# Optimization experiments

Measured on AMD Instinct MI355X. Metric: run time of the kernel, lower is better.

Reference implementation:

```python
import jax, jax.numpy as jnp
import numpy as np

DIM = 2048
HEADS = 16
KV_HEADS = 4
DIM_HEAD = 128
INNER = HEADS * DIM_HEAD          # 2048
KV_INNER = KV_HEADS * DIM_HEAD    # 512
FF = 4 * DIM                      # 8192
QK_SCALE = 10.0                   # x-transformers default qk_norm_scale
B, S = 2, 2048


def layer_norm(x, g, b, eps=1e-5):
    m = jnp.mean(x, axis=-1, keepdims=True)
    v = jnp.mean((x - m) ** 2, axis=-1, keepdims=True)
    return (x - m) * jax.lax.rsqrt(v + eps) * g + b


def l2norm(t, eps=1e-12):
    n = jnp.sqrt(jnp.sum(t * t, axis=-1, keepdims=True))
    return t / jnp.maximum(n, eps)


def setup_inputs() -> dict:
    key = jax.random.key(0)
    ks = jax.random.split(key, 12)
    s = lambda fan_in: 1.0 / np.sqrt(fan_in)
    return {
        "x":     jax.random.normal(ks[0], (B, S, DIM), jnp.float32),
        "wq":    jax.random.normal(ks[1], (DIM, INNER), jnp.float32) * s(DIM),
        "wk":    jax.random.normal(ks[2], (DIM, KV_INNER), jnp.float32) * s(DIM),
        "wv":    jax.random.normal(ks[3], (DIM, KV_INNER), jnp.float32) * s(DIM),
        "wo":    jax.random.normal(ks[4], (INNER, DIM), jnp.float32) * s(INNER),
        "ln1_g": jnp.ones((DIM,), jnp.float32),
        "ln1_b": jnp.zeros((DIM,), jnp.float32),
        "w1":    jax.random.normal(ks[5], (DIM, FF), jnp.float32) * s(DIM),
        "b1":    jnp.zeros((FF,), jnp.float32),
        "lnf_g": jnp.ones((FF,), jnp.float32),
        "lnf_b": jnp.zeros((FF,), jnp.float32),
        "w2":    jax.random.normal(ks[6], (FF, DIM), jnp.float32) * s(FF),
        "b2":    jnp.zeros((DIM,), jnp.float32),
    }


def reference(x, wq, wk, wv, wo, ln1_g, ln1_b, w1, b1, lnf_g, lnf_b, w2, b2):
    b, s, _ = x.shape
    rep = HEADS // KV_HEADS
    # GQA projections
    q = (x @ wq).reshape(b, s, HEADS, DIM_HEAD).transpose(0, 2, 1, 3)      # [b,h,s,d]
    k = (x @ wk).reshape(b, s, KV_HEADS, DIM_HEAD).transpose(0, 2, 1, 3)   # [b,g,s,d]
    v = (x @ wv).reshape(b, s, KV_HEADS, DIM_HEAD).transpose(0, 2, 1, 3)
    # qk-norm: l2-normalize q/k along head dim, fixed scale
    q = l2norm(q)
    k = l2norm(k)
    k = jnp.repeat(k, rep, axis=1)  # expand kv heads to query heads
    v = jnp.repeat(v, rep, axis=1)
    scores = jnp.einsum("bhid,bhjd->bhij", q, k) * QK_SCALE
    attn = jax.nn.softmax(scores, axis=-1)
    o = jnp.einsum("bhij,bhjd->bhid", attn, v)
    o = o.transpose(0, 2, 1, 3).reshape(b, s, INNER) @ wo
    # post-attention LayerNorm (no residual in the source)
    h = layer_norm(o, ln1_g, ln1_b)
    # FFN: SiLU + post-activation LayerNorm (dropout inert in eval)
    f = jax.nn.silu(h @ w1 + b1)
    f = layer_norm(f, lnf_g, lnf_b)
    y = f @ w2 + b2
    # the source re-applies the SAME norm after the ffn
    return layer_norm(y, ln1_g, ln1_b)
```

## Files before the change

### kernel.cpp

```cpp
#include <hip/hip_runtime.h>


typedef __attribute__((ext_vector_type(8))) short short8;
typedef __attribute__((ext_vector_type(4))) float f32x4;
typedef __attribute__((ext_vector_type(16))) float f32x16;

__device__ __forceinline__ unsigned short f2bf(float f) {
  unsigned int u = __builtin_bit_cast(unsigned int, f);
  u += 0x7FFFu + ((u >> 16) & 1u);
  return (unsigned short)(u >> 16);
}
__device__ __forceinline__ float bf2f(unsigned short h) {
  unsigned int u = ((unsigned int)h) << 16;
  return __builtin_bit_cast(float, u);
}

typedef const void __attribute__((address_space(1)))* gas1_t;
typedef void __attribute__((address_space(3)))* las3_t;
#define GLDS16(g, l) \
  __builtin_amdgcn_global_load_lds((gas1_t)(const void*)(g), (las3_t)(void*)(l), 16, 0, 0)

__global__ __launch_bounds__(256) void cast_f32_bf16(const float* __restrict__ src,
                                                     unsigned short* __restrict__ dst,
                                                     int n) {
  int i = (blockIdx.x * 256 + threadIdx.x) * 4;
  if (i >= n) return;
  float4 f = *(const float4*)(src + i);
  uint2 u;
  u.x = (unsigned)f2bf(f.x) | ((unsigned)f2bf(f.y) << 16);
  u.y = (unsigned)f2bf(f.z) | ((unsigned)f2bf(f.w) << 16);
  *(uint2*)(dst + i) = u;
}

__global__ void transcast(const float* __restrict__ src, unsigned short* __restrict__ dst,
                          int R, int C, int dst_ld, int row_off) {
  __shared__ float t[32][33];
  const int tx = threadIdx.x, ty = threadIdx.y;
  const int c0 = blockIdx.x * 32, r0 = blockIdx.y * 32;
#pragma unroll
  for (int j = 0; j < 4; ++j)
    t[ty + j * 8][tx] = src[(size_t)(r0 + ty + j * 8) * C + c0 + tx];
  __syncthreads();
#pragma unroll
  for (int j = 0; j < 4; ++j)
    dst[(size_t)(row_off + c0 + ty + j * 8) * dst_ld + r0 + tx] = f2bf(t[tx][ty + j * 8]);
}

template <int BN>
__global__ __launch_bounds__(512, 2) void gemm256(const unsigned short* __restrict__ A,
                                                  const unsigned short* __restrict__ Bt,
                                                  unsigned short* __restrict__ C,
                                                  int M, int N, int K) {
  constexpr int NF = BN / 64;
  constexpr int HB = BN * 64;
  constexpr int RB = BN / 128;
  constexpr int AK1 = 16384 + HB;
  constexpr int BUFB = 32768 + 2 * HB;
  extern __shared__ char lds[];

  const int tid = threadIdx.x, l = tid & 63, w = tid >> 6;
  const int wr = w >> 2, wc = w & 3;
  const int brow = blockIdx.y * 256, bcol = blockIdx.x * BN;
  const unsigned short* Aa = A + (size_t)brow * K;
  const unsigned short* Bb = Bt + (size_t)bcol * K;
  const int NT = K >> 6;

  const int slot = l >> 4;
  const int rowA = wr * 128 + (l & 15);
  const int aRd = ((((rowA << 2) | slot) << 4) ^ ((rowA & 7) << 4));
  const int rowB = wc * (BN / 4) + (l & 15);
  const int bRd = ((((rowB << 2) | slot) << 4) ^ ((rowB & 7) << 4));

  f32x4 acc[8][NF];
#pragma unroll
  for (int m = 0; m < 8; ++m)
#pragma unroll
    for (int n = 0; n < NF; ++n) acc[m][n] = (f32x4){0.f, 0.f, 0.f, 0.f};

  auto stageA = [&](char* dst, int kofs) {
#pragma unroll
    for (int r = 0; r < 2; ++r) {
      const int g = r * 512 + tid;
      const int rw = ((g >> 3) << 1) | (((g >> 2) ^ (g >> 4)) & 1);
      const int sl = (g ^ rw) & 3;
      GLDS16(Aa + (size_t)rw * K + kofs + sl * 8, dst + g * 16);
    }
  };
  auto stageB = [&](char* dst, int kofs) {
#pragma unroll
    for (int r = 0; r < RB; ++r) {
      const int g = r * 512 + tid;
      const int rw = ((g >> 3) << 1) | (((g >> 2) ^ (g >> 4)) & 1);
      const int sl = (g ^ rw) & 3;
      GLDS16(Bb + (size_t)rw * K + kofs + sl * 8, dst + g * 16);
    }
  };

  stageA(lds, 0);
  stageB(lds + 16384, 0);
  stageA(lds + AK1, 32);
  stageB(lds + AK1 + 16384, 32);

  int kt = 0;
  for (int t = 0; t < NT; ++t) {
    char* curb = lds + (t & 1) * BUFB;
    char* nxtb = lds + ((t & 1) ^ 1) * BUFB;
    const int ktn = (t + 1 < NT) ? kt + 64 : 0;
    short8 af[4], bf[NF];

    if constexpr (BN == 256) asm volatile("s_waitcnt vmcnt(4)" ::: "memory");
    else                     asm volatile("s_waitcnt vmcnt(3)" ::: "memory");
    asm volatile("s_barrier" ::: "memory");
#pragma unroll
    for (int n = 0; n < NF; ++n) bf[n] = *(const short8*)(curb + 16384 + bRd + n * 1024);
#pragma unroll
    for (int m = 0; m < 4; ++m) af[m] = *(const short8*)(curb + aRd + m * 1024);
    stageA(nxtb, ktn);
    __builtin_amdgcn_s_setprio(1);
#pragma unroll
    for (int m = 0; m < 4; ++m)
#pragma unroll
      for (int n = 0; n < NF; ++n)
        acc[m][n] = __builtin_amdgcn_mfma_f32_16x16x32_bf16(af[m], bf[n], acc[m][n], 0, 0, 0);
    __builtin_amdgcn_s_setprio(0);

    asm volatile("s_barrier" ::: "memory");
#pragma unroll
    for (int m = 0; m < 4; ++m) af[m] = *(const short8*)(curb + aRd + (m + 4) * 1024);
    stageB(nxtb + 16384, ktn);
    __builtin_amdgcn_s_setprio(1);
#pragma unroll
    for (int m = 0; m < 4; ++m)
#pragma unroll
      for (int n = 0; n < NF; ++n)
        acc[m + 4][n] = __builtin_amdgcn_mfma_f32_16x16x32_bf16(af[m], bf[n], acc[m + 4][n], 0, 0, 0);
    __builtin_amdgcn_s_setprio(0);

    if constexpr (BN == 256) asm volatile("s_waitcnt vmcnt(4)" ::: "memory");
    else                     asm volatile("s_waitcnt vmcnt(3)" ::: "memory");
    asm volatile("s_barrier" ::: "memory");
#pragma unroll
    for (int n = 0; n < NF; ++n) bf[n] = *(const short8*)(curb + AK1 + 16384 + bRd + n * 1024);
#pragma unroll
    for (int m = 0; m < 4; ++m) af[m] = *(const short8*)(curb + AK1 + aRd + m * 1024);
    stageA(nxtb + AK1, ktn + 32);
    __builtin_amdgcn_s_setprio(1);
#pragma unroll
    for (int m = 0; m < 4; ++m)
#pragma unroll
      for (int n = 0; n < NF; ++n)
        acc[m][n] = __builtin_amdgcn_mfma_f32_16x16x32_bf16(af[m], bf[n], acc[m][n], 0, 0, 0);
    __builtin_amdgcn_s_setprio(0);

    asm volatile("s_barrier" ::: "memory");
#pragma unroll
    for (int m = 0; m < 4; ++m) af[m] = *(const short8*)(curb + AK1 + aRd + (m + 4) * 1024);
    stageB(nxtb + AK1 + 16384, ktn + 32);
    __builtin_amdgcn_s_setprio(1);
#pragma unroll
    for (int m = 0; m < 4; ++m)
#pragma unroll
      for (int n = 0; n < NF; ++n)
        acc[m + 4][n] = __builtin_amdgcn_mfma_f32_16x16x32_bf16(af[m], bf[n], acc[m + 4][n], 0, 0, 0);
    __builtin_amdgcn_s_setprio(0);

    kt += 64;
  }

#pragma unroll
  for (int m = 0; m < 8; ++m)
#pragma unroll
    for (int r = 0; r < 4; ++r) {
      const int row = brow + wr * 128 + m * 16 + (l >> 4) * 4 + r;
#pragma unroll
      for (int n = 0; n < NF; ++n) {
        const int col = bcol + wc * (BN / 4) + n * 16 + (l & 15);
        C[(size_t)row * N + col] = f2bf(acc[m][n][r]);
      }
    }
}

__global__ __launch_bounds__(256) void l2norm_qk(unsigned short* __restrict__ qkv) {
  const int wid = blockIdx.x * 4 + (threadIdx.x >> 6);
  const int l = threadIdx.x & 63;
  const int token = wid / 20, u = wid % 20;
  const int col = (u < 16) ? u * 128 : 2048 + (u - 16) * 128;
  unsigned short* p = qkv + (size_t)token * 3072 + col + l * 2;
  const float a = bf2f(p[0]), b = bf2f(p[1]);
  float ss = a * a + b * b;
#pragma unroll
  for (int m = 1; m < 64; m <<= 1) ss += __shfl_xor(ss, m);
  const float sc = ((u < 16) ? 10.f : 1.f) / fmaxf(sqrtf(ss), 1e-12f);
  p[0] = f2bf(a * sc);
  p[1] = f2bf(b * sc);
}

__global__ __launch_bounds__(256) void vtrans(const unsigned short* __restrict__ qkv,
                                              unsigned short* __restrict__ vt) {
  const int idx = blockIdx.x * 256 + threadIdx.x;
  const int s_ = idx & 2047;
  const int rest = idx >> 11;
  const int d = rest & 127;
  const int bg = rest >> 7;
  const int b = bg >> 2, g = bg & 3;
  vt[idx] = qkv[(size_t)(b * 2048 + s_) * 3072 + 2560 + g * 128 + d];
}

__global__ __launch_bounds__(512) void attn_kernel(const unsigned short* __restrict__ qkv,
                                                   const unsigned short* __restrict__ vt,
                                                   unsigned short* __restrict__ out) {
  extern __shared__ char smem[];
  const int tid = threadIdx.x, w = tid >> 6, l = tid & 63;
  const int hi = l >> 5, l31 = l & 31;

  const int n = blockIdx.x;
  const int np = (n & 7) * 32 + (n >> 3);
  const int qi = np & 7, bh = np >> 3;
  const int b = bh >> 4, h = bh & 15, g = h >> 2;
  const int q0 = qi * 256;

  const unsigned short* kbase = qkv + (size_t)(b * 2048) * 3072 + 2048 + g * 128;
  const unsigned short* vbase = vt + (size_t)(b * 4 + g) * 128 * 2048;

  short8 qf[8];
  {
    const unsigned short* qrow = qkv + (size_t)(b * 2048 + q0 + w * 32 + l31) * 3072 + h * 128;
#pragma unroll
    for (int st = 0; st < 8; ++st)
      qf[st] = *(const short8*)&qrow[st * 16 + hi * 8];
  }

  f32x16 o[4];
#pragma unroll
  for (int d0 = 0; d0 < 4; ++d0)
#pragma unroll
    for (int i = 0; i < 16; ++i) o[d0][i] = 0.f;
  float l_part = 0.f;

  const int krow = tid >> 3, kc = (tid & 7) * 2;
  const int vd = tid >> 2, vc = (tid & 3) * 2;
  const unsigned short* kg = kbase + (size_t)krow * 3072 + kc * 8;
  const unsigned short* vg = vbase + (size_t)vd * 2048 + vc * 8;
  const int ko0 = krow * 256 + ((kc ^ (krow & 15)) << 4);
  const int ko1 = krow * 256 + (((kc + 1) ^ (krow & 15)) << 4);
  const int vrp = vd >> 1, vcl = (vd & 1) * 8;
  const int vo0 = vrp * 256 + (((vcl + vc) ^ (vrp & 15)) << 4);
  const int vo1 = vrp * 256 + (((vcl + vc + 1) ^ (vrp & 15)) << 4);

  {
    uint4 k0 = *(const uint4*)kg, k1 = *(const uint4*)(kg + 8);
    uint4 v0 = *(const uint4*)vg, v1 = *(const uint4*)(vg + 8);
    char* Kb = smem;
    char* Vb = smem + 16384;
    *(uint4*)(Kb + ko0) = k0; *(uint4*)(Kb + ko1) = k1;
    *(uint4*)(Vb + vo0) = v0; *(uint4*)(Vb + vo1) = v1;
  }
  __syncthreads();

  const int swzk = l31 & 15;
  for (int t = 0; t < 32; ++t) {
    uint4 k0, k1, v0, v1;
    const bool more = (t + 1) < 32;
    if (more) {
      const size_t kvo = (size_t)(t + 1) * 64;
      k0 = *(const uint4*)(kg + kvo * 3072);
      k1 = *(const uint4*)(kg + kvo * 3072 + 8);
      v0 = *(const uint4*)(vg + kvo);
      v1 = *(const uint4*)(vg + kvo + 8);
    }

    char* Kb = smem + (t & 1) * 32768;
    char* Vb = Kb + 16384;

    f32x16 s0, s1;
#pragma unroll
    for (int i = 0; i < 16; ++i) { s0[i] = 0.f; s1[i] = 0.f; }
    __builtin_amdgcn_s_setprio(1);
#pragma unroll
    for (int st = 0; st < 8; ++st) {
      const int ch = st * 2 + hi;
      short8 kf0 = *(const short8*)(Kb + l31 * 256 + ((ch ^ swzk) << 4));
      short8 kf1 = *(const short8*)(Kb + (l31 + 32) * 256 + ((ch ^ swzk) << 4));
      s0 = __builtin_amdgcn_mfma_f32_32x32x16_bf16(kf0, qf[st], s0, 0, 0, 0);
      s1 = __builtin_amdgcn_mfma_f32_32x32x16_bf16(kf1, qf[st], s1, 0, 0, 0);
    }
    __builtin_amdgcn_s_setprio(0);

#pragma unroll
    for (int i = 0; i < 16; ++i) {
      s0[i] = __expf(s0[i] - 10.f);
      s1[i] = __expf(s1[i] - 10.f);
      l_part += s0[i] + s1[i];
    }

    short8 pa[4];
#pragma unroll
    for (int ks = 0; ks < 4; ++ks) {
      const f32x16& sv = (ks < 2) ? s0 : s1;
      const int base = (ks & 1) * 8;
      auto pk = [](float x, float y) -> unsigned {
        unsigned ux = __builtin_bit_cast(unsigned, x);
        unsigned uy = __builtin_bit_cast(unsigned, y);
        return ((uy + 0x8000u) & 0xFFFF0000u) | ((ux + 0x8000u) >> 16);
      };
      unsigned a = pk(sv[base + 0], sv[base + 1]);
      unsigned bq = pk(sv[base + 4], sv[base + 5]);
      unsigned c = pk(sv[base + 2], sv[base + 3]);
      unsigned d = pk(sv[base + 6], sv[base + 7]);
      unsigned as = __shfl_xor(a, 32), bs = __shfl_xor(bq, 32);
      unsigned cs = __shfl_xor(c, 32), ds = __shfl_xor(d, 32);
      uint4 wv;
      wv.x = (l < 32) ? a : bs;
      wv.y = (l < 32) ? c : ds;
      wv.z = (l < 32) ? as : bq;
      wv.w = (l < 32) ? cs : d;
      pa[ks] = __builtin_bit_cast(short8, wv);
    }

    __builtin_amdgcn_s_setprio(1);
#pragma unroll
    for (int ks = 0; ks < 4; ++ks) {
#pragma unroll
      for (int d0 = 0; d0 < 4; ++d0) {
        const int dd = d0 * 32 + l31;
        const int rp = dd >> 1;
        const int cl = ((dd & 1) * 8 + ks * 2 + hi) ^ (rp & 15);
        short8 vf = *(const short8*)(Vb + rp * 256 + (cl << 4));
        o[d0] = __builtin_amdgcn_mfma_f32_32x32x16_bf16(pa[ks], vf, o[d0], 0, 0, 0);
      }
    }
    __builtin_amdgcn_s_setprio(0);

    __syncthreads();
    if (more) {
      char* Kn = smem + ((t + 1) & 1) * 32768;
      char* Vn = Kn + 16384;
      *(uint4*)(Kn + ko0) = k0; *(uint4*)(Kn + ko1) = k1;
      *(uint4*)(Vn + vo0) = v0; *(uint4*)(Vn + vo1) = v1;
    }
    __syncthreads();
  }

  float ltot = l_part + __shfl_xor(l_part, 32);
  float linv = 1.f / ltot;
  const int tok_base = b * 2048 + q0 + w * 32;
#pragma unroll
  for (int r = 0; r < 16; ++r) {
    const int qr = (r & 3) + 8 * (r >> 2) + 4 * hi;
    const float li = __shfl(linv, qr);
    unsigned short* orow = out + (size_t)(tok_base + qr) * 2048 + h * 128 + l31;
#pragma unroll
    for (int d0 = 0; d0 < 4; ++d0)
      orow[d0 * 32] = f2bf(o[d0][r] * li);
  }
}

template <int NC, bool BIAS, bool SILU, bool OUTF32>
__global__ __launch_bounds__(256) void ln_row(const unsigned short* __restrict__ src,
                                              unsigned short* __restrict__ dstb,
                                              float* __restrict__ dstf,
                                              const float* __restrict__ gamma,
                                              const float* __restrict__ beta,
                                              const float* __restrict__ bias) {
  constexpr int E = NC / 256;
  const int row = blockIdx.x, tid = threadIdx.x;
  const size_t base = (size_t)row * NC + tid * E;
  float v[E];
#pragma unroll
  for (int c = 0; c < E / 8; ++c) {
    uint4 u = *(const uint4*)(src + base + c * 8);
    const unsigned short* us = (const unsigned short*)&u;
#pragma unroll
    for (int j = 0; j < 8; ++j) v[c * 8 + j] = bf2f(us[j]);
  }
  if constexpr (BIAS) {
#pragma unroll
    for (int i = 0; i < E; ++i) v[i] += bias[tid * E + i];
  }
  if constexpr (SILU) {
#pragma unroll
    for (int i = 0; i < E; ++i) v[i] = v[i] / (1.f + __expf(-v[i]));
  }
  float s = 0.f, q = 0.f;
#pragma unroll
  for (int i = 0; i < E; ++i) {
    s += v[i];
    q += v[i] * v[i];
  }
#pragma unroll
  for (int m = 1; m < 64; m <<= 1) {
    s += __shfl_xor(s, m);
    q += __shfl_xor(q, m);
  }
  __shared__ float rs[4], rq[4];
  if ((tid & 63) == 0) {
    rs[tid >> 6] = s;
    rq[tid >> 6] = q;
  }
  __syncthreads();
  s = rs[0] + rs[1] + rs[2] + rs[3];
  q = rq[0] + rq[1] + rq[2] + rq[3];
  const float mean = s / NC;
  const float rstd = rsqrtf(q / NC - mean * mean + 1e-5f);
#pragma unroll
  for (int i = 0; i < E; ++i)
    v[i] = (v[i] - mean) * rstd * gamma[tid * E + i] + beta[tid * E + i];
  if constexpr (OUTF32) {
#pragma unroll
    for (int c = 0; c < E / 4; ++c) {
      float4 f = {v[c * 4], v[c * 4 + 1], v[c * 4 + 2], v[c * 4 + 3]};
      *(float4*)(dstf + base + c * 4) = f;
    }
  } else {
#pragma unroll
    for (int c = 0; c < E / 8; ++c) {
      uint4 u;
      unsigned* up = (unsigned*)&u;
#pragma unroll
      for (int j = 0; j < 4; ++j)
        up[j] = (unsigned)f2bf(v[c * 8 + j * 2]) | ((unsigned)f2bf(v[c * 8 + j * 2 + 1]) << 16);
      *(uint4*)(dstb + base + c * 8) = u;
    }
  }
}

extern "C" void kernel_launch(void* const* d_in, const int* in_sizes, int n_in,
                              void* d_out, int out_size, void* d_ws, size_t ws_size,
                              hipStream_t stream) {
  (void)in_sizes; (void)n_in; (void)out_size; (void)ws_size;
  const float* x     = (const float*)d_in[0];
  const float* wq    = (const float*)d_in[1];
  const float* wk    = (const float*)d_in[2];
  const float* wv    = (const float*)d_in[3];
  const float* wo    = (const float*)d_in[4];
  const float* ln1_g = (const float*)d_in[5];
  const float* ln1_b = (const float*)d_in[6];
  const float* w1    = (const float*)d_in[7];
  const float* b1    = (const float*)d_in[8];
  const float* lnf_g = (const float*)d_in[9];
  const float* lnf_b = (const float*)d_in[10];
  const float* w2    = (const float*)d_in[11];
  const float* b2    = (const float*)d_in[12];

  unsigned short* ws = (unsigned short*)d_ws;
  unsigned short* wqkvT  = ws;
  unsigned short* woT    = wqkvT  + (size_t)3072 * 2048;
  unsigned short* w1T    = woT    + (size_t)2048 * 2048;
  unsigned short* w2T    = w1T    + (size_t)8192 * 2048;
  unsigned short* xb     = w2T    + (size_t)2048 * 8192;
  unsigned short* qkv    = xb     + (size_t)4096 * 2048;
  unsigned short* vt     = qkv    + (size_t)4096 * 3072;
  unsigned short* attn_o = vt     + (size_t)4096 * 512;
  unsigned short* f1     = attn_o + (size_t)4096 * 2048;

  (void)hipFuncSetAttribute((const void*)gemm256<256>,
                            hipFuncAttributeMaxDynamicSharedMemorySize, 131072);
  (void)hipFuncSetAttribute((const void*)gemm256<128>,
                            hipFuncAttributeMaxDynamicSharedMemorySize, 98304);
  (void)hipFuncSetAttribute((const void*)attn_kernel,
                            hipFuncAttributeMaxDynamicSharedMemorySize, 65536);

  const dim3 tb(32, 8);
  cast_f32_bf16<<<8192, 256, 0, stream>>>(x, xb, 4096 * 2048);
  transcast<<<dim3(64, 64),  tb, 0, stream>>>(wq, wqkvT, 2048, 2048, 2048, 0);
  transcast<<<dim3(16, 64),  tb, 0, stream>>>(wk, wqkvT, 2048, 512, 2048, 2048);
  transcast<<<dim3(16, 64),  tb, 0, stream>>>(wv, wqkvT, 2048, 512, 2048, 2560);
  transcast<<<dim3(64, 64),  tb, 0, stream>>>(wo, woT, 2048, 2048, 2048, 0);
  transcast<<<dim3(256, 64), tb, 0, stream>>>(w1, w1T, 2048, 8192, 2048, 0);
  transcast<<<dim3(64, 256), tb, 0, stream>>>(w2, w2T, 8192, 2048, 8192, 0);

  gemm256<256><<<dim3(12, 16), 512, 131072, stream>>>(xb, wqkvT, qkv, 4096, 3072, 2048);
  l2norm_qk<<<20480, 256, 0, stream>>>(qkv);
  vtrans<<<8192, 256, 0, stream>>>(qkv, vt);
  attn_kernel<<<256, 512, 65536, stream>>>(qkv, vt, attn_o);
  gemm256<128><<<dim3(16, 16), 512, 98304, stream>>>(attn_o, woT, xb, 4096, 2048, 2048);
  ln_row<2048, false, false, false><<<4096, 256, 0, stream>>>(xb, xb, nullptr, ln1_g, ln1_b, nullptr);
  gemm256<256><<<dim3(32, 16), 512, 131072, stream>>>(xb, w1T, f1, 4096, 8192, 2048);
  ln_row<8192, true, true, false><<<4096, 256, 0, stream>>>(f1, f1, nullptr, lnf_g, lnf_b, b1);
  gemm256<128><<<dim3(16, 16), 512, 98304, stream>>>(f1, w2T, qkv, 4096, 2048, 8192);
  ln_row<2048, true, false, true><<<4096, 256, 0, stream>>>(qkv, nullptr, (float*)d_out, ln1_g, ln1_b, b2);
}
```

Before: 651.3 us.

## Add triple-buffered 256x128 GEMM with XCD-aware tile mapping for N=2048 GEMMs

Adds a gemm128r3 kernel that uses three LDS buffers (144KB, one block per CU) to prefetch two K-steps ahead, and replaces gemm256<128> for the Wo and W2 projections with it. Both the new kernel and gemm256 now remap block IDs so that blocks sharing an XCD work on nearby tiles, to improve L2 reuse of A and B. The deeper pipeline hides global-load latency but halves occupancy relative to the 2-blocks-per-CU variant. The remap in gemm256 assumes the grid size is divisible by 8.

Measured after the change: 645.0 us. No clear change (-1.0%).

```diff
diff --git a/kernel.cpp b/kernel.cpp
--- a/kernel.cpp
+++ b/kernel.cpp
@@ -60,7 +60,11 @@
 
   const int tid = threadIdx.x, l = tid & 63, w = tid >> 6;
   const int wr = w >> 2, wc = w & 3;
-  const int brow = blockIdx.y * 256, bcol = blockIdx.x * BN;
+  const int gx = gridDim.x, gy = gridDim.y;
+  const int did = blockIdx.y * gx + blockIdx.x;
+  const int q = (gx * gy) >> 3;
+  const int tcm = (did & 7) * q + (did >> 3);
+  const int brow = (tcm % gy) * 256, bcol = (tcm / gy) * BN;
   const unsigned short* Aa = A + (size_t)brow * K;
   const unsigned short* Bb = Bt + (size_t)bcol * K;
   const int NT = K >> 6;
@@ -175,6 +179,135 @@
 #pragma unroll
       for (int n = 0; n < NF; ++n) {
         const int col = bcol + wc * (BN / 4) + n * 16 + (l & 15);
+        C[(size_t)row * N + col] = f2bf(acc[m][n][r]);
+      }
+    }
+}
+
+__global__ __launch_bounds__(512, 1) void gemm128r3(const unsigned short* __restrict__ A,
+                                                    const unsigned short* __restrict__ Bt,
+                                                    unsigned short* __restrict__ C,
+                                                    int M, int N, int K) {
+  constexpr int BUFB = 49152;
+  extern __shared__ char lds[];
+  const int tid = threadIdx.x, l = tid & 63, w = tid >> 6;
+  const int wr = w >> 2, wc = w & 3;
+  const int did = blockIdx.y * 16 + blockIdx.x;
+  const int xcd = did & 7, idx = did >> 3;
+  const int brow = ((xcd >> 1) * 4 + (idx & 3)) * 256;
+  const int bcol = ((xcd & 1) * 8 + (idx >> 2)) * 128;
+  const unsigned short* Aa = A + (size_t)brow * K;
+  const unsigned short* Bb = Bt + (size_t)bcol * K;
+  const int NT = K >> 6;
+
+  const int slot = l >> 4;
+  const int rowA = wr * 128 + (l & 15);
+  const int aRd = ((((rowA << 2) | slot) << 4) ^ ((rowA & 7) << 4));
+  const int rowB = wc * 32 + (l & 15);
+  const int bRd = ((((rowB << 2) | slot) << 4) ^ ((rowB & 7) << 4));
+
+  f32x4 acc[8][2];
+#pragma unroll
+  for (int m = 0; m < 8; ++m)
+#pragma unroll
+    for (int n = 0; n < 2; ++n) acc[m][n] = (f32x4){0.f, 0.f, 0.f, 0.f};
+
+  auto stageA = [&](char* dst, int kofs) {
+#pragma unroll
+    for (int r = 0; r < 2; ++r) {
+      const int g = r * 512 + tid;
+      const int rw = ((g >> 3) << 1) | (((g >> 2) ^ (g >> 4)) & 1);
+      const int sl = (g ^ rw) & 3;
+      GLDS16(Aa + (size_t)rw * K + kofs + sl * 8, dst + g * 16);
+    }
+  };
+  auto stageB = [&](char* dst, int kofs) {
+    const int g = tid;
+    const int rw = ((g >> 3) << 1) | (((g >> 2) ^ (g >> 4)) & 1);
+    const int sl = (g ^ rw) & 3;
+    GLDS16(Bb + (size_t)rw * K + kofs + sl * 8, dst + g * 16);
+  };
+
+  stageA(lds, 0);                  stageB(lds + 16384, 0);
+  stageA(lds + 24576, 32);         stageB(lds + 40960, 32);
+  stageA(lds + BUFB, 64);          stageB(lds + BUFB + 16384, 64);
+  stageA(lds + BUFB + 24576, 96);  stageB(lds + BUFB + 40960, 96);
+
+  char* b0 = lds;
+  char* b1 = lds + BUFB;
+  char* b2 = lds + 2 * BUFB;
+  int kt2 = 128;
+  for (int t = 0; t < NT; ++t) {
+    char* cur = b0;
+    char* nxt = b2;
+    const int kn = (t + 2 < NT) ? kt2 : 0;
+    short8 af[4], bf[2];
+
+    asm volatile("s_waitcnt vmcnt(6)" ::: "memory");
+    asm volatile("s_barrier" ::: "memory");
+    bf[0] = *(const short8*)(cur + 16384 + bRd);
+    bf[1] = *(const short8*)(cur + 16384 + bRd + 1024);
+#pragma unroll
+    for (int m = 0; m < 4; ++m) af[m] = *(const short8*)(cur + aRd + m * 1024);
+    stageA(nxt, kn);
+    stageB(nxt + 16384, kn);
+    __builtin_amdgcn_s_setprio(1);
+#pragma unroll
+    for (int m = 0; m < 4; ++m)
+#pragma unroll
+      for (int n = 0; n < 2; ++n)
+        acc[m][n] = __builtin_amdgcn_mfma_f32_16x16x32_bf16(af[m], bf[n], acc[m][n], 0, 0, 0);
+    __builtin_amdgcn_s_setprio(0);
+
+    asm volatile("s_barrier" ::: "memory");
+#pragma unroll
+    for (int m = 0; m < 4; ++m) af[m] = *(const short8*)(cur + aRd + (m + 4) * 1024);
+    stageA(nxt + 24576, kn + 32);
+    stageB(nxt + 40960, kn + 32);
+    __builtin_amdgcn_s_setprio(1);
+#pragma unroll
+    for (int m = 0; m < 4; ++m)
+#pragma unroll
+      for (int n = 0; n < 2; ++n)
+        acc[m + 4][n] = __builtin_amdgcn_mfma_f32_16x16x32_bf16(af[m], bf[n], acc[m + 4][n], 0, 0, 0);
+    __builtin_amdgcn_s_setprio(0);
+
+    asm volatile("s_barrier" ::: "memory");
+    bf[0] = *(const short8*)(cur + 40960 + bRd);
+    bf[1] = *(const short8*)(cur + 40960 + bRd + 1024);
+#pragma unroll
+    for (int m = 0; m < 4; ++m) af[m] = *(const short8*)(cur + 24576 + aRd + m * 1024);
+    __builtin_amdgcn_s_setprio(1);
+#pragma unroll
+    for (int m = 0; m < 4; ++m)
+#pragma unroll
+      for (int n = 0; n < 2; ++n)
+        acc[m][n] = __builtin_amdgcn_mfma_f32_16x16x32_bf16(af[m], bf[n], acc[m][n], 0, 0, 0);
+    __builtin_amdgcn_s_setprio(0);
+
+    asm volatile("s_barrier" ::: "memory");
+#pragma unroll
+    for (int m = 0; m < 4; ++m) af[m] = *(const short8*)(cur + 24576 + aRd + (m + 4) * 1024);
+    __builtin_amdgcn_s_setprio(1);
+#pragma unroll
+    for (int m = 0; m < 4; ++m)
+#pragma unroll
+      for (int n = 0; n < 2; ++n)
+        acc[m + 4][n] = __builtin_amdgcn_mfma_f32_16x16x32_bf16(af[m], bf[n], acc[m + 4][n], 0, 0, 0);
+    __builtin_amdgcn_s_setprio(0);
+
+    char* tmp = b0; b0 = b1; b1 = b2; b2 = tmp;
+    kt2 += 64;
+  }
+
+#pragma unroll
+  for (int m = 0; m < 8; ++m)
+#pragma unroll
+    for (int r = 0; r < 4; ++r) {
+      const int row = brow + wr * 128 + m * 16 + (l >> 4) * 4 + r;
+#pragma unroll
+      for (int n = 0; n < 2; ++n) {
+        const int col = bcol + wc * 32 + n * 16 + (l & 15);
         C[(size_t)row * N + col] = f2bf(acc[m][n][r]);
       }
     }
@@ -455,8 +588,8 @@
 
   (void)hipFuncSetAttribute((const void*)gemm256<256>,
                             hipFuncAttributeMaxDynamicSharedMemorySize, 131072);
-  (void)hipFuncSetAttribute((const void*)gemm256<128>,
-                            hipFuncAttributeMaxDynamicSharedMemorySize, 98304);
+  (void)hipFuncSetAttribute((const void*)gemm128r3,
+                            hipFuncAttributeMaxDynamicSharedMemorySize, 147456);
   (void)hipFuncSetAttribute((const void*)attn_kernel,
                             hipFuncAttributeMaxDynamicSharedMemorySize, 65536);
 
@@ -473,10 +606,10 @@
   l2norm_qk<<<20480, 256, 0, stream>>>(qkv);
   vtrans<<<8192, 256, 0, stream>>>(qkv, vt);
   attn_kernel<<<256, 512, 65536, stream>>>(qkv, vt, attn_o);
-  gemm256<128><<<dim3(16, 16), 512, 98304, stream>>>(attn_o, woT, xb, 4096, 2048, 2048);
+  gemm128r3<<<dim3(16, 16), 512, 147456, stream>>>(attn_o, woT, xb, 4096, 2048, 2048);
   ln_row<2048, false, false, false><<<4096, 256, 0, stream>>>(xb, xb, nullptr, ln1_g, ln1_b, nullptr);
   gemm256<256><<<dim3(32, 16), 512, 131072, stream>>>(xb, w1T, f1, 4096, 8192, 2048);
   ln_row<8192, true, true, false><<<4096, 256, 0, stream>>>(f1, f1, nullptr, lnf_g, lnf_b, b1);
-  gemm256<128><<<dim3(16, 16), 512, 98304, stream>>>(f1, w2T, qkv, 4096, 2048, 8192);
+  gemm128r3<<<dim3(16, 16), 512, 147456, stream>>>(f1, w2T, qkv, 4096, 2048, 8192);
   ln_row<2048, true, false, true><<<4096, 256, 0, stream>>>(qkv, nullptr, (float*)d_out, ln1_g, ln1_b, b2);
 }
```

## Rewrite GEMM as 8-phase pipelined 256x256 tile with XCD remap and split-K

Applied to the files above, without the earlier changes.

Replaces the two-tile-width GEMM with one 256x256-tile kernel that streams four 16KB stages per k-tile through a deeper prefetch schedule (six stages in flight), with barriers placed around each MFMA phase. Block IDs are remapped so that consecutive tiles land on the same XCD, aiming for better L2 reuse. The N=2048 GEMMs (wo, w2) now use split-K=2 over the z grid dimension, producing two bf16 partials that the following LayerNorm kernel sums, so the grid fills more CUs. This costs extra partial-output traffic, rounds each partial to bf16 before summing, and drops to one block per CU because of the 128KB LDS.

Measured after the change: 672.0 us. 3.2% more time.

```diff
diff --git a/kernel.cpp b/kernel.cpp
--- a/kernel.cpp
+++ b/kernel.cpp
@@ -46,125 +46,83 @@
     dst[(size_t)(row_off + c0 + ty + j * 8) * dst_ld + r0 + tx] = f2bf(t[tx][ty + j * 8]);
 }
 
-template <int BN>
-__global__ __launch_bounds__(512, 2) void gemm256(const unsigned short* __restrict__ A,
+template <int KS>
+__global__ __launch_bounds__(512, 1) void gemm8ph(const unsigned short* __restrict__ A,
                                                   const unsigned short* __restrict__ Bt,
-                                                  unsigned short* __restrict__ C,
-                                                  int M, int N, int K) {
-  constexpr int NF = BN / 64;
-  constexpr int HB = BN * 64;
-  constexpr int RB = BN / 128;
-  constexpr int AK1 = 16384 + HB;
-  constexpr int BUFB = 32768 + 2 * HB;
+                                                  unsigned short* __restrict__ C0,
+                                                  unsigned short* __restrict__ C1,
+                                                  int ldc, int Keff) {
   extern __shared__ char lds[];
-
   const int tid = threadIdx.x, l = tid & 63, w = tid >> 6;
   const int wr = w >> 2, wc = w & 3;
-  const int brow = blockIdx.y * 256, bcol = blockIdx.x * BN;
-  const unsigned short* Aa = A + (size_t)brow * K;
-  const unsigned short* Bb = Bt + (size_t)bcol * K;
-  const int NT = K >> 6;
+  const int gx = gridDim.x, gy = gridDim.y;
+  const int did = blockIdx.y * gx + blockIdx.x;
+  const int q = (gx * gy) >> 3;
+  const int tcm = (did & 7) * q + (did >> 3);
+  const int brow = (tcm % gy) * 256, bcol = (tcm / gy) * 256;
+  const int ld = Keff * KS;
+  const unsigned short* Aa = A + (size_t)brow * ld + blockIdx.z * Keff;
+  const unsigned short* Bb = Bt + (size_t)bcol * ld + blockIdx.z * Keff;
+  unsigned short* C = (KS == 1 || blockIdx.z == 0) ? C0 : C1;
+  const int NT = Keff >> 6;
 
   const int slot = l >> 4;
   const int rowA = wr * 128 + (l & 15);
   const int aRd = ((((rowA << 2) | slot) << 4) ^ ((rowA & 7) << 4));
-  const int rowB = wc * (BN / 4) + (l & 15);
+  const int rowB = wc * 64 + (l & 15);
   const int bRd = ((((rowB << 2) | slot) << 4) ^ ((rowB & 7) << 4));
 
-  f32x4 acc[8][NF];
+  f32x4 acc[8][4];
 #pragma unroll
   for (int m = 0; m < 8; ++m)
 #pragma unroll
-    for (int n = 0; n < NF; ++n) acc[m][n] = (f32x4){0.f, 0.f, 0.f, 0.f};
-
-  auto stageA = [&](char* dst, int kofs) {
+    for (int n = 0; n < 4; ++n) acc[m][n] = (f32x4){0.f, 0.f, 0.f, 0.f};
+
+  auto stage = [&](int s) {
+    const int tile = s >> 2, kind = s & 3;
+    const int kofs = ((tile < NT) ? tile * 64 : 0) + (kind >> 1) * 32;
+    const unsigned short* src = (kind & 1) ? Bb : Aa;
+    char* dst = lds + (tile & 1) * 65536 + kind * 16384;
 #pragma unroll
     for (int r = 0; r < 2; ++r) {
       const int g = r * 512 + tid;
       const int rw = ((g >> 3) << 1) | (((g >> 2) ^ (g >> 4)) & 1);
       const int sl = (g ^ rw) & 3;
-      GLDS16(Aa + (size_t)rw * K + kofs + sl * 8, dst + g * 16);
+      GLDS16(src + (size_t)rw * ld + kofs + sl * 8, dst + g * 16);
     }
   };
-  auto stageB = [&](char* dst, int kofs) {
-#pragma unroll
-    for (int r = 0; r < RB; ++r) {
-      const int g = r * 512 + tid;
-      const int rw = ((g >> 3) << 1) | (((g >> 2) ^ (g >> 4)) & 1);
-      const int sl = (g ^ rw) & 3;
-      GLDS16(Bb + (size_t)rw * K + kofs + sl * 8, dst + g * 16);
-    }
-  };
-
-  stageA(lds, 0);
-  stageB(lds + 16384, 0);
-  stageA(lds + AK1, 32);
-  stageB(lds + AK1 + 16384, 32);
-
-  int kt = 0;
-  for (int t = 0; t < NT; ++t) {
-    char* curb = lds + (t & 1) * BUFB;
-    char* nxtb = lds + ((t & 1) ^ 1) * BUFB;
-    const int ktn = (t + 1 < NT) ? kt + 64 : 0;
-    short8 af[4], bf[NF];
-
-    if constexpr (BN == 256) asm volatile("s_waitcnt vmcnt(4)" ::: "memory");
-    else                     asm volatile("s_waitcnt vmcnt(3)" ::: "memory");
-    asm volatile("s_barrier" ::: "memory");
-#pragma unroll
-    for (int n = 0; n < NF; ++n) bf[n] = *(const short8*)(curb + 16384 + bRd + n * 1024);
-#pragma unroll
-    for (int m = 0; m < 4; ++m) af[m] = *(const short8*)(curb + aRd + m * 1024);
-    stageA(nxtb, ktn);
-    __builtin_amdgcn_s_setprio(1);
-#pragma unroll
-    for (int m = 0; m < 4; ++m)
-#pragma unroll
-      for (int n = 0; n < NF; ++n)
-        acc[m][n] = __builtin_amdgcn_mfma_f32_16x16x32_bf16(af[m], bf[n], acc[m][n], 0, 0, 0);
-    __builtin_amdgcn_s_setprio(0);
-
-    asm volatile("s_barrier" ::: "memory");
-#pragma unroll
-    for (int m = 0; m < 4; ++m) af[m] = *(const short8*)(curb + aRd + (m + 4) * 1024);
-    stageB(nxtb + 16384, ktn);
-    __builtin_amdgcn_s_setprio(1);
-#pragma unroll
-    for (int m = 0; m < 4; ++m)
-#pragma unroll
-      for (int n = 0; n < NF; ++n)
-        acc[m + 4][n] = __builtin_amdgcn_mfma_f32_16x16x32_bf16(af[m], bf[n], acc[m + 4][n], 0, 0, 0);
-    __builtin_amdgcn_s_setprio(0);
-
-    if constexpr (BN == 256) asm volatile("s_waitcnt vmcnt(4)" ::: "memory");
-    else                     asm volatile("s_waitcnt vmcnt(3)" ::: "memory");
-    asm volatile("s_barrier" ::: "memory");
-#pragma unroll
-    for (int n = 0; n < NF; ++n) bf[n] = *(const short8*)(curb + AK1 + 16384 + bRd + n * 1024);
-#pragma unroll
-    for (int m = 0; m < 4; ++m) af[m] = *(const short8*)(curb + AK1 + aRd + m * 1024);
-    stageA(nxtb + AK1, ktn + 32);
-    __builtin_amdgcn_s_setprio(1);
-#pragma unroll
-    for (int m = 0; m < 4; ++m)
-#pragma unroll
-      for (int n = 0; n < NF; ++n)
-        acc[m][n] = __builtin_amdgcn_mfma_f32_16x16x32_bf16(af[m], bf[n], acc[m][n], 0, 0, 0);
-    __builtin_amdgcn_s_setprio(0);
-
-    asm volatile("s_barrier" ::: "memory");
-#pragma unroll
-    for (int m = 0; m < 4; ++m) af[m] = *(const short8*)(curb + AK1 + aRd + (m + 4) * 1024);
-    stageB(nxtb + AK1 + 16384, ktn + 32);
-    __builtin_amdgcn_s_setprio(1);
-#pragma unroll
-    for (int m = 0; m < 4; ++m)
-#pragma unroll
-      for (int n = 0; n < NF; ++n)
-        acc[m + 4][n] = __builtin_amdgcn_mfma_f32_16x16x32_bf16(af[m], bf[n], acc[m + 4][n], 0, 0, 0);
-    __builtin_amdgcn_s_setprio(0);
-
-    kt += 64;
+
+  stage(0); stage(1); stage(2); stage(3); stage(4); stage(5);
+  asm volatile("s_waitcnt vmcnt(4)" ::: "memory");
+  __builtin_amdgcn_s_barrier();
+
+  for (int T = 0; T < NT; ++T) {
+    char* cur = lds + (T & 1) * 65536;
+#pragma unroll
+    for (int ph = 0; ph < 4; ++ph) {
+      const int ks = ph >> 1, mh = ph & 1;
+      char* abase = cur + ks * 32768;
+      char* bbase = cur + 16384 + ks * 32768;
+      short8 af[4], bf[4];
+#pragma unroll
+      for (int n = 0; n < 4; ++n) bf[n] = *(const short8*)(bbase + bRd + n * 1024);
+#pragma unroll
+      for (int m = 0; m < 4; ++m) af[m] = *(const short8*)(abase + aRd + (mh * 4 + m) * 1024);
+      stage(4 * T + ph + 6);
+      __builtin_amdgcn_s_barrier();
+      asm volatile("s_waitcnt lgkmcnt(0)" ::: "memory");
+      __builtin_amdgcn_sched_barrier(0);
+      __builtin_amdgcn_s_setprio(1);
+#pragma unroll
+      for (int m = 0; m < 4; ++m)
+#pragma unroll
+        for (int n = 0; n < 4; ++n)
+          acc[mh * 4 + m][n] =
+              __builtin_amdgcn_mfma_f32_16x16x32_bf16(af[m], bf[n], acc[mh * 4 + m][n], 0, 0, 0);
+      __builtin_amdgcn_s_setprio(0);
+      if (ph == 3) asm volatile("s_waitcnt vmcnt(4)" ::: "memory");
+      __builtin_amdgcn_s_barrier();
+    }
   }
 
 #pragma unroll
@@ -173,9 +131,9 @@
     for (int r = 0; r < 4; ++r) {
       const int row = brow + wr * 128 + m * 16 + (l >> 4) * 4 + r;
 #pragma unroll
-      for (int n = 0; n < NF; ++n) {
-        const int col = bcol + wc * (BN / 4) + n * 16 + (l & 15);
-        C[(size_t)row * N + col] = f2bf(acc[m][n][r]);
+      for (int n = 0; n < 4; ++n) {
+        const int col = bcol + wc * 64 + n * 16 + (l & 15);
+        C[(size_t)row * ldc + col] = f2bf(acc[m][n][r]);
       }
     }
 }
@@ -355,8 +313,9 @@
   }
 }
 
-template <int NC, bool BIAS, bool SILU, bool OUTF32>
+template <int NC, bool BIAS, bool SILU, bool OUTF32, bool SUM2>
 __global__ __launch_bounds__(256) void ln_row(const unsigned short* __restrict__ src,
+                                              const unsigned short* __restrict__ src2,
                                               unsigned short* __restrict__ dstb,
                                               float* __restrict__ dstf,
                                               const float* __restrict__ gamma,
@@ -372,6 +331,15 @@
     const unsigned short* us = (const unsigned short*)&u;
 #pragma unroll
     for (int j = 0; j < 8; ++j) v[c * 8 + j] = bf2f(us[j]);
+  }
+  if constexpr (SUM2) {
+#pragma unroll
+    for (int c = 0; c < E / 8; ++c) {
+      uint4 u = *(const uint4*)(src2 + base + c * 8);
+      const unsigned short* us = (const unsigned short*)&u;
+#pragma unroll
+      for (int j = 0; j < 8; ++j) v[c * 8 + j] += bf2f(us[j]);
+    }
   }
   if constexpr (BIAS) {
 #pragma unroll
@@ -453,10 +421,10 @@
   unsigned short* attn_o = vt     + (size_t)4096 * 512;
   unsigned short* f1     = attn_o + (size_t)4096 * 2048;
 
-  (void)hipFuncSetAttribute((const void*)gemm256<256>,
+  (void)hipFuncSetAttribute((const void*)gemm8ph<1>,
                             hipFuncAttributeMaxDynamicSharedMemorySize, 131072);
-  (void)hipFuncSetAttribute((const void*)gemm256<128>,
-                            hipFuncAttributeMaxDynamicSharedMemorySize, 98304);
+  (void)hipFuncSetAttribute((const void*)gemm8ph<2>,
+                            hipFuncAttributeMaxDynamicSharedMemorySize, 131072);
   (void)hipFuncSetAttribute((const void*)attn_kernel,
                             hipFuncAttributeMaxDynamicSharedMemorySize, 65536);
 
@@ -469,14 +437,17 @@
   transcast<<<dim3(256, 64), tb, 0, stream>>>(w1, w1T, 2048, 8192, 2048, 0);
   transcast<<<dim3(64, 256), tb, 0, stream>>>(w2, w2T, 8192, 2048, 8192, 0);
 
-  gemm256<256><<<dim3(12, 16), 512, 131072, stream>>>(xb, wqkvT, qkv, 4096, 3072, 2048);
+  gemm8ph<1><<<dim3(12, 16, 1), 512, 131072, stream>>>(xb, wqkvT, qkv, nullptr, 3072, 2048);
   l2norm_qk<<<20480, 256, 0, stream>>>(qkv);
   vtrans<<<8192, 256, 0, stream>>>(qkv, vt);
   attn_kernel<<<256, 512, 65536, stream>>>(qkv, vt, attn_o);
-  gemm256<128><<<dim3(16, 16), 512, 98304, stream>>>(attn_o, woT, xb, 4096, 2048, 2048);
-  ln_row<2048, false, false, false><<<4096, 256, 0, stream>>>(xb, xb, nullptr, ln1_g, ln1_b, nullptr);
-  gemm256<256><<<dim3(32, 16), 512, 131072, stream>>>(xb, w1T, f1, 4096, 8192, 2048);
-  ln_row<8192, true, true, false><<<4096, 256, 0, stream>>>(f1, f1, nullptr, lnf_g, lnf_b, b1);
-  gemm256<128><<<dim3(16, 16), 512, 98304, stream>>>(f1, w2T, qkv, 4096, 2048, 8192);
-  ln_row<2048, true, false, true><<<4096, 256, 0, stream>>>(qkv, nullptr, (float*)d_out, ln1_g, ln1_b, b2);
-}
+  gemm8ph<2><<<dim3(8, 16, 2), 512, 131072, stream>>>(attn_o, woT, qkv, f1, 2048, 1024);
+  ln_row<2048, false, false, false, true><<<4096, 256, 0, stream>>>(
+      qkv, f1, xb, nullptr, ln1_g, ln1_b, nullptr);
+  gemm8ph<1><<<dim3(32, 16, 1), 512, 131072, stream>>>(xb, w1T, f1, nullptr, 8192, 2048);
+  ln_row<8192, true, true, false, false><<<4096, 256, 0, stream>>>(
+      f1, nullptr, f1, nullptr, lnf_g, lnf_b, b1);
+  gemm8ph<2><<<dim3(8, 16, 2), 512, 131072, stream>>>(f1, w2T, xb, attn_o, 2048, 4096);
+  ln_row<2048, true, false, true, true><<<4096, 256, 0, stream>>>(
+      xb, attn_o, nullptr, (float*)d_out, ln1_g, ln1_b, b2);
+}
```
